# Optimization experiments

Measured on AMD Instinct MI355X. Metric: run time of the kernel, lower is better.

Reference implementation:

```python
import jax, jax.numpy as jnp
import numpy as np

N, D, R, T, E = 4096, 1024, 92, 32, 8192
SCALE = float(np.sqrt(2.0 / 7.0))  # matches torch.rand(...) * sqrt(2/7)


def setup_inputs() -> dict:
    key = jax.random.key(0)
    ks = jax.random.split(key, 7)
    x = jax.random.normal(ks[0], (N, D), dtype=jnp.float32)
    edge_tok = jax.random.randint(ks[1], (E,), 0, N)
    edge_rel = jax.random.randint(ks[2], (E,), 0, R)
    W_stack = jax.random.uniform(ks[3], (R, D, D), dtype=jnp.float32) * SCALE  # depWeights
    B_stack = jnp.ones((R, D), dtype=jnp.float32)                              # depBias
    W_self = jax.random.uniform(ks[4], (D, D), dtype=jnp.float32) * SCALE      # self.weight
    b_self = jnp.ones((D,), dtype=jnp.float32)                                 # self.bias
    W_tag = jax.random.normal(ks[5], (D, T), dtype=jnp.float32) * 0.02         # hidden2tag
    b_tag = jnp.zeros((T,), dtype=jnp.float32)
    return {"x": x, "W_self": W_self, "b_self": b_self, "W_stack": W_stack,
            "B_stack": B_stack, "W_tag": W_tag, "b_tag": b_tag,
            "edge_tok": edge_tok, "edge_rel": edge_rel}


def reference(x, W_self, b_self, W_stack, B_stack, W_tag, b_tag, edge_tok, edge_rel):
    n, r = x.shape[0], W_stack.shape[0]
    # C[i, r] = number of dependency edges of token i with relation r
    C = jnp.zeros((n, r), dtype=x.dtype).at[edge_tok, edge_rel].add(jnp.asarray(1.0, x.dtype))
    self_out = x @ W_self + b_self  # [N, D]
    # accum_i = self_out_i + sum_{dep in deps(i)} (x_i @ W_dep + b_dep)
    #         = self_out_i + sum_r C[i, r] * (x_i @ W_r) + (C @ B_stack)_i
    def body(acc, wc):
        Wr, Cr = wc  # Wr: [D, D], Cr: [N]
        return acc + Cr[:, None] * (x @ Wr), None
    dep_out, _ = jax.lax.scan(body, jnp.zeros_like(self_out), (W_stack, C.T))
    h = jax.nn.relu(self_out + dep_out + C @ B_stack)  # [N, D]
    tag_scores = jax.nn.log_softmax(h @ W_tag + b_tag, axis=1)  # [N, T]
    return tag_scores, h
```

## Files before the change

### kernel.cpp

```cpp
#include <hip/hip_runtime.h>
#include <hip/hip_bf16.h>
#include <math.h>

#define N_TOK 4096
#define D_DIM 1024
#define R_REL 92
#define T_TAG 32
#define E_EDGE 8192
#define SELF_R 127
#define GRID_ITEMS 192


typedef short bf16x8 __attribute__((ext_vector_type(8)));
typedef float f32x4 __attribute__((ext_vector_type(4)));

union Pk8 { uint4 q; unsigned short s[8]; };
union Pk4 { uint2 d; unsigned short s[4]; };

__device__ __forceinline__ unsigned short f2bf(float f) {
    union { __hip_bfloat16 b; unsigned short u; } c;
    c.b = __float2bfloat16(f);
    return c.u;
}
__device__ __forceinline__ float bf2f(unsigned short u) {
    return __uint_as_float(((unsigned)u) << 16);
}

__global__ __launch_bounds__(1024) void k_setup(const int* __restrict__ rel,
                                                const int* __restrict__ tokv,
                                                int* __restrict__ ws) {
    __shared__ int cnt[128], offL[128], cur[128];
    __shared__ int sh[128];
    __shared__ int wsum[16];
    __shared__ int tcnt[4096], toff[4096];
    int t = threadIdx.x;
    int lane = t & 63, wid = t >> 6;
    if (t < 128) { cnt[t] = 0; cur[t] = 0; }
    #pragma unroll
    for (int i = 0; i < 4; ++i) tcnt[i * 1024 + t] = 0;
    __syncthreads();
    int er[8], et[8];
    #pragma unroll
    for (int i = 0; i < 8; ++i) {
        er[i] = rel[i * 1024 + t];
        et[i] = tokv[i * 1024 + t];
        atomicAdd(&cnt[er[i]], 1);
        atomicAdd(&tcnt[et[i]], 1);
    }
    __syncthreads();
    int c = (t < 128) ? cnt[t] : 0;
    int v = c;
    if (t < 128) sh[t] = v;
    __syncthreads();
    for (int st = 1; st < 128; st <<= 1) {
        int add = (t >= st && t < 128) ? sh[t - st] : 0;
        __syncthreads();
        if (t < 128) { v += add; sh[t] = v; }
        __syncthreads();
    }
    if (t < 128) { offL[t] = v - c; ws[256 + t] = v - c; ws[t] = c; }
    int ch = (t < R_REL) ? ((c + 127) >> 7) : 0;
    int v2 = ch;
    if (t < 128) sh[t] = v2;
    __syncthreads();
    for (int st = 1; st < 128; st <<= 1) {
        int add = (t >= st && t < 128) ? sh[t - st] : 0;
        __syncthreads();
        if (t < 128) { v2 += add; sh[t] = v2; }
        __syncthreads();
    }
    if (t < 32) ws[512 + t] = (SELF_R << 16) | t;
    if (t < R_REL) {
        int excl = v2 - ch;
        for (int j = 0; j < ch; ++j)
            ws[512 + 32 + excl + j] = (t << 16) | j;
    }
    if (t == 127) ws[384] = 32 + v2;
    int s0 = tcnt[4 * t + 0], s1 = tcnt[4 * t + 1];
    int s2 = tcnt[4 * t + 2], s3 = tcnt[4 * t + 3];
    int sum4 = s0 + s1 + s2 + s3;
    int vv = sum4;
    #pragma unroll
    for (int d = 1; d < 64; d <<= 1) {
        int n = __shfl_up(vv, d);
        if (lane >= d) vv += n;
    }
    if (lane == 63) wsum[wid] = vv;
    __syncthreads();
    if (wid == 0) {
        int wv = (lane < 16) ? wsum[lane] : 0;
        #pragma unroll
        for (int d = 1; d < 16; d <<= 1) {
            int n = __shfl_up(wv, d);
            if (lane >= d) wv += n;
        }
        if (lane < 16) wsum[lane] = wv;
    }
    __syncthreads();
    int base = (wid > 0) ? wsum[wid - 1] : 0;
    int incl = base + vv;
    int ex = incl - sum4;
    toff[4 * t + 0] = ex;
    toff[4 * t + 1] = ex + s0;
    toff[4 * t + 2] = ex + s0 + s1;
    toff[4 * t + 3] = ex + s0 + s1 + s2;
    ws[17408 + 4 * t + 0] = ex;
    ws[17408 + 4 * t + 1] = ex + s0;
    ws[17408 + 4 * t + 2] = ex + s0 + s1;
    ws[17408 + 4 * t + 3] = ex + s0 + s1 + s2;
    if (t == 1023) ws[17408 + 4096] = incl;
    __syncthreads();
    #pragma unroll
    for (int i = 0; i < 4; ++i) tcnt[i * 1024 + t] = 0;
    __syncthreads();
    #pragma unroll
    for (int i = 0; i < 8; ++i) {
        int pos = offL[er[i]] + atomicAdd(&cur[er[i]], 1);
        ws[1024 + pos] = et[i];
        int q = toff[et[i]] + atomicAdd(&tcnt[et[i]], 1);
        ws[22528 + q] = pos;
    }
}

__global__ __launch_bounds__(256, 2) void k_fused(const float* __restrict__ x,
                                                  const float* __restrict__ Wself,
                                                  const float* __restrict__ bself,
                                                  const float* __restrict__ Wst,
                                                  const float* __restrict__ Bst,
                                                  const int* __restrict__ ws,
                                                  unsigned short* __restrict__ scratch) {
    if ((int)blockIdx.x >= ws[384]) return;
    int item = ws[512 + blockIdx.x];
    int r = item >> 16, chunk = item & 0xFFFF;
    int m0 = chunk * 128;
    int valid;
    const float* Wbase;
    const float* bias;
    bool is_self = (r == SELF_R);
    int off0 = 0;
    if (is_self) {
        valid = 128;
        Wbase = Wself;
        bias = bself;
    } else {
        int cnt = ws[r];
        off0 = ws[256 + r];
        valid = cnt - m0; if (valid > 128) valid = 128;
        Wbase = Wst + (size_t)r * D_DIM * D_DIM;
        bias = Bst + (size_t)r * D_DIM;
    }
    int srow_base = is_self ? (8192 + m0) : (off0 + m0);

    __shared__ unsigned short Al[2][128 * 64];
    __shared__ unsigned short Bl[2][128 * 64];
    __shared__ int toks[128];
    int t = threadIdx.x;
    if (t < 128) {
        int tok;
        if (is_self) tok = m0 + t;
        else tok = (t < valid) ? ws[1024 + off0 + m0 + t] : 0;
        toks[t] = tok;
    }
    __syncthreads();

    int gn0 = blockIdx.y * 128;
    int w = t >> 6, l = t & 63;
    int lr = l & 15, lg = l >> 4;
    int wm = (w >> 1) * 64, wn = (w & 1) * 64;
    int ar = t >> 4, ac = t & 15;
    int tok_s[8];
    #pragma unroll
    for (int s = 0; s < 8; ++s) tok_s[s] = toks[s * 16 + ar];
    int bn = (w & 1) * 64 + l;
    int bkb = (w >> 1) * 32;
    const float* wcol = Wbase + gn0 + bn;

    float4 pa[8];
    float pb[32];

    #pragma unroll
    for (int s = 0; s < 8; ++s)
        pa[s] = *(const float4*)(x + (size_t)tok_s[s] * D_DIM + ac * 4);
    #pragma unroll
    for (int s = 0; s < 4; ++s)
        #pragma unroll
        for (int i = 0; i < 8; ++i)
            pb[s * 8 + i] = wcol[(size_t)(bkb + s * 8 + i) * D_DIM];
    {
        char* Ab = (char*)Al[0];
        char* Bb = (char*)Bl[0];
        #pragma unroll
        for (int s = 0; s < 8; ++s) {
            int row = s * 16 + ar;
            Pk4 u;
            u.s[0] = f2bf(pa[s].x); u.s[1] = f2bf(pa[s].y);
            u.s[2] = f2bf(pa[s].z); u.s[3] = f2bf(pa[s].w);
            *(uint2*)(Ab + row * 128 + ((ac * 8) ^ ((row & 7) << 4))) = u.d;
        }
        #pragma unroll
        for (int s = 0; s < 4; ++s) {
            Pk8 u;
            #pragma unroll
            for (int i = 0; i < 8; ++i) u.s[i] = f2bf(pb[s * 8 + i]);
            *(uint4*)(Bb + bn * 128 + ((bkb * 2 + s * 16) ^ ((bn & 7) << 4))) = u.q;
        }
    }
    __syncthreads();

    f32x4 acc[4][4] = {};
    int cur = 0;
    for (int k0 = 0; k0 < D_DIM; k0 += 64) {
        bool pf = (k0 + 64 < D_DIM);
        if (pf) {
            int kn = k0 + 64;
            #pragma unroll
            for (int s = 0; s < 8; ++s)
                pa[s] = *(const float4*)(x + (size_t)tok_s[s] * D_DIM + kn + ac * 4);
            #pragma unroll
            for (int s = 0; s < 4; ++s)
                #pragma unroll
                for (int i = 0; i < 8; ++i)
                    pb[s * 8 + i] = wcol[(size_t)(kn + bkb + s * 8 + i) * D_DIM];
        }
        char* Ac = (char*)Al[cur];
        char* Bc = (char*)Bl[cur];
        #pragma unroll
        for (int kk = 0; kk < 2; ++kk) {
            int koff = kk * 64 + lg * 16;
            bf16x8 af[4], bfr[4];
            #pragma unroll
            for (int mi = 0; mi < 4; ++mi)
                af[mi] = *(const bf16x8*)(Ac + (wm + mi * 16 + lr) * 128 +
                                          (koff ^ ((lr & 7) << 4)));
            #pragma unroll
            for (int ni = 0; ni < 4; ++ni)
                bfr[ni] = *(const bf16x8*)(Bc + (wn + ni * 16 + lr) * 128 +
                                           (koff ^ ((lr & 7) << 4)));
            #pragma unroll
            for (int mi = 0; mi < 4; ++mi)
                #pragma unroll
                for (int ni = 0; ni < 4; ++ni)
                    acc[mi][ni] = __builtin_amdgcn_mfma_f32_16x16x32_bf16(
                        af[mi], bfr[ni], acc[mi][ni], 0, 0, 0);
        }
        if (pf) {
            char* An = (char*)Al[cur ^ 1];
            char* Bn = (char*)Bl[cur ^ 1];
            #pragma unroll
            for (int s = 0; s < 8; ++s) {
                int row = s * 16 + ar;
                Pk4 u;
                u.s[0] = f2bf(pa[s].x); u.s[1] = f2bf(pa[s].y);
                u.s[2] = f2bf(pa[s].z); u.s[3] = f2bf(pa[s].w);
                *(uint2*)(An + row * 128 + ((ac * 8) ^ ((row & 7) << 4))) = u.d;
            }
            #pragma unroll
            for (int s = 0; s < 4; ++s) {
                Pk8 u;
                #pragma unroll
                for (int i = 0; i < 8; ++i) u.s[i] = f2bf(pb[s * 8 + i]);
                *(uint4*)(Bn + bn * 128 + ((bkb * 2 + s * 16) ^ ((bn & 7) << 4))) = u.q;
            }
        }
        __syncthreads();
        cur ^= 1;
    }
    float bb[4];
    #pragma unroll
    for (int ni = 0; ni < 4; ++ni) bb[ni] = bias[gn0 + wn + ni * 16 + lr];
    #pragma unroll
    for (int mi = 0; mi < 4; ++mi)
        #pragma unroll
        for (int j = 0; j < 4; ++j) {
            int rl = wm + mi * 16 + lg * 4 + j;
            if (rl < valid) {
                unsigned short* dst = scratch +
                    (size_t)(srow_base + rl) * D_DIM + gn0 + wn + lr;
                #pragma unroll
                for (int ni = 0; ni < 4; ++ni)
                    dst[ni * 16] = f2bf(acc[mi][ni][j] + bb[ni]);
            }
        }
}

__global__ __launch_bounds__(256) void k_reduce(const int* __restrict__ ws,
                                                const unsigned short* __restrict__ scratch,
                                                float* __restrict__ out_h) {
    int tok = blockIdx.x;
    int t = threadIdx.x;
    int j0 = ws[17408 + tok], j1 = ws[17408 + tok + 1];
    ushort4 sv = *(const ushort4*)(scratch + (size_t)(8192 + tok) * D_DIM + t * 4);
    float a0 = bf2f(sv.x), a1 = bf2f(sv.y), a2 = bf2f(sv.z), a3 = bf2f(sv.w);
    for (int j = j0; j < j1; ++j) {
        int p = ws[22528 + j];
        ushort4 dv = *(const ushort4*)(scratch + (size_t)p * D_DIM + t * 4);
        a0 += bf2f(dv.x); a1 += bf2f(dv.y); a2 += bf2f(dv.z); a3 += bf2f(dv.w);
    }
    float4 o;
    o.x = fmaxf(a0, 0.f); o.y = fmaxf(a1, 0.f);
    o.z = fmaxf(a2, 0.f); o.w = fmaxf(a3, 0.f);
    *(float4*)(out_h + (size_t)tok * D_DIM + t * 4) = o;
}

__global__ __launch_bounds__(256) void k_tag(const float* __restrict__ out_h,
                                             const float* __restrict__ Wt,
                                             const float* __restrict__ bt,
                                             float* __restrict__ out_tag) {
    __shared__ unsigned short Al[64 * 64];
    __shared__ unsigned short Bl[32 * 64];
    char* Alb = (char*)Al;
    char* Blb = (char*)Bl;
    int tok0 = blockIdx.x * 64;
    int t = threadIdx.x;
    int w = t >> 6, l = t & 63, lr = l & 15, lg = l >> 4;
    int wm = w * 16;
    int ar = t >> 4, ac = t & 15;
    int bn = t & 31, kh = t >> 5;
    f32x4 acc[2] = {};
    for (int k0 = 0; k0 < D_DIM; k0 += 64) {
        __syncthreads();
        #pragma unroll
        for (int s = 0; s < 4; ++s) {
            int row = s * 16 + ar;
            const float* hp = out_h + (size_t)(tok0 + row) * D_DIM + k0 + ac * 4;
            float4 v = *(const float4*)hp;
            Pk4 u;
            u.s[0] = f2bf(v.x); u.s[1] = f2bf(v.y);
            u.s[2] = f2bf(v.z); u.s[3] = f2bf(v.w);
            *(uint2*)(Alb + row * 128 + ((ac * 8) ^ ((row & 7) << 4))) = u.d;
        }
        {
            Pk8 u;
            #pragma unroll
            for (int i = 0; i < 8; ++i)
                u.s[i] = f2bf(Wt[(size_t)(k0 + kh * 8 + i) * T_TAG + bn]);
            *(uint4*)(Blb + bn * 128 + ((kh * 16) ^ ((bn & 7) << 4))) = u.q;
        }
        __syncthreads();
        #pragma unroll
        for (int kk = 0; kk < 2; ++kk) {
            int koff = kk * 64 + lg * 16;
            bf16x8 af = *(const bf16x8*)(Alb + (wm + lr) * 128 +
                                         (koff ^ ((lr & 7) << 4)));
            #pragma unroll
            for (int ni = 0; ni < 2; ++ni) {
                bf16x8 bfr = *(const bf16x8*)(Blb + (ni * 16 + lr) * 128 +
                                              (koff ^ ((lr & 7) << 4)));
                acc[ni] = __builtin_amdgcn_mfma_f32_16x16x32_bf16(
                    af, bfr, acc[ni], 0, 0, 0);
            }
        }
    }
    float bt0 = bt[lr], bt1 = bt[16 + lr];
    #pragma unroll
    for (int j = 0; j < 4; ++j) {
        float v0 = acc[0][j] + bt0;
        float v1 = acc[1][j] + bt1;
        float m = fmaxf(v0, v1);
        #pragma unroll
        for (int s = 1; s < 16; s <<= 1) m = fmaxf(m, __shfl_xor(m, s));
        float sum = expf(v0 - m) + expf(v1 - m);
        #pragma unroll
        for (int s = 1; s < 16; s <<= 1) sum += __shfl_xor(sum, s);
        float lse = m + logf(sum);
        int row = tok0 + wm + lg * 4 + j;
        out_tag[(size_t)row * T_TAG + lr] = v0 - lse;
        out_tag[(size_t)row * T_TAG + 16 + lr] = v1 - lse;
    }
}

extern "C" void kernel_launch(void* const* d_in, const int* in_sizes, int n_in,
                              void* d_out, int out_size, void* d_ws, size_t ws_size,
                              hipStream_t stream) {
    const float* x     = (const float*)d_in[0];
    const float* Wself = (const float*)d_in[1];
    const float* bself = (const float*)d_in[2];
    const float* Wst   = (const float*)d_in[3];
    const float* Bst   = (const float*)d_in[4];
    const float* Wtag  = (const float*)d_in[5];
    const float* btag  = (const float*)d_in[6];
    const int*   etok  = (const int*)d_in[7];
    const int*   erel  = (const int*)d_in[8];
    float* out_tag = (float*)d_out;
    float* out_h   = (float*)d_out + (size_t)N_TOK * T_TAG;
    int* ws = (int*)d_ws;
    unsigned short* scratch = (unsigned short*)((int*)d_ws + 32768);

    k_setup<<<1, 1024, 0, stream>>>(erel, etok, ws);
    k_fused<<<dim3(GRID_ITEMS, D_DIM / 128), 256, 0, stream>>>(
        x, Wself, bself, Wst, Bst, ws, scratch);
    k_reduce<<<N_TOK, 256, 0, stream>>>(ws, scratch, out_h);
    k_tag<<<N_TOK / 64, 256, 0, stream>>>(out_h, Wtag, btag, out_tag);
}
```

Before: 149.4 us.

## Pre-convert x to bf16 and stream A tiles via direct global-to-LDS loads

Adds blocks to the setup kernel that convert x to a bf16 copy in workspace, so the GEMM kernel can gather token rows with global_load_lds straight into swizzled shared memory instead of loading fp32 into registers and converting. The GEMM block grows from 256 to 512 threads with an 8-wave 2x4 layout (each wave computes 64x32), which halves per-thread B loads and accumulators and raises the occupancy hint. This removes register staging and conversion work for A in the main loop, at the cost of an extra pass over x and more waves sharing LDS and barriers.

```diff
diff --git a/kernel.cpp b/kernel.cpp
--- a/kernel.cpp
+++ b/kernel.cpp
@@ -25,15 +25,34 @@
 __device__ __forceinline__ float bf2f(unsigned short u) {
     return __uint_as_float(((unsigned)u) << 16);
 }
-
-__global__ __launch_bounds__(1024) void k_setup(const int* __restrict__ rel,
-                                                const int* __restrict__ tokv,
-                                                int* __restrict__ ws) {
+__device__ __forceinline__ void gload_lds16(const void* g, void* l) {
+    __builtin_amdgcn_global_load_lds(
+        (const __attribute__((address_space(1))) unsigned int*)g,
+        (__attribute__((address_space(3))) unsigned int*)l, 16, 0, 0);
+}
+
+__global__ __launch_bounds__(1024) void k_prep(const int* __restrict__ rel,
+                                               const int* __restrict__ tokv,
+                                               const float* __restrict__ x,
+                                               int* __restrict__ ws,
+                                               unsigned short* __restrict__ xb) {
+    int t = threadIdx.x;
+    if (blockIdx.x > 0) {
+        size_t base = ((size_t)(blockIdx.x - 1) * 1024 + t) * 8;
+        float4 v0 = *(const float4*)(x + base);
+        float4 v1 = *(const float4*)(x + base + 4);
+        Pk8 u;
+        u.s[0] = f2bf(v0.x); u.s[1] = f2bf(v0.y);
+        u.s[2] = f2bf(v0.z); u.s[3] = f2bf(v0.w);
+        u.s[4] = f2bf(v1.x); u.s[5] = f2bf(v1.y);
+        u.s[6] = f2bf(v1.z); u.s[7] = f2bf(v1.w);
+        *(uint4*)(xb + base) = u.q;
+        return;
+    }
     __shared__ int cnt[128], offL[128], cur[128];
     __shared__ int sh[128];
     __shared__ int wsum[16];
     __shared__ int tcnt[4096], toff[4096];
-    int t = threadIdx.x;
     int lane = t & 63, wid = t >> 6;
     if (t < 128) { cnt[t] = 0; cur[t] = 0; }
     #pragma unroll
@@ -122,12 +141,12 @@
     }
 }
 
-__global__ __launch_bounds__(256, 2) void k_fused(const float* __restrict__ x,
-                                                  const float* __restrict__ Wself,
+__global__ __launch_bounds__(512, 4) void k_fused(const float* __restrict__ Wself,
                                                   const float* __restrict__ bself,
                                                   const float* __restrict__ Wst,
                                                   const float* __restrict__ Bst,
                                                   const int* __restrict__ ws,
+                                                  const unsigned short* __restrict__ xb,
                                                   unsigned short* __restrict__ scratch) {
     if ((int)blockIdx.x >= ws[384]) return;
     int item = ws[512 + blockIdx.x];
@@ -151,8 +170,8 @@
     }
     int srow_base = is_self ? (8192 + m0) : (off0 + m0);
 
-    __shared__ unsigned short Al[2][128 * 64];
-    __shared__ unsigned short Bl[2][128 * 64];
+    __shared__ unsigned short Al[2][8192];
+    __shared__ unsigned short Bl[2][8192];
     __shared__ int toks[128];
     int t = threadIdx.x;
     if (t < 128) {
@@ -164,110 +183,84 @@
     __syncthreads();
 
     int gn0 = blockIdx.y * 128;
-    int w = t >> 6, l = t & 63;
+    int wid = t >> 6, l = t & 63;
     int lr = l & 15, lg = l >> 4;
-    int wm = (w >> 1) * 64, wn = (w & 1) * 64;
-    int ar = t >> 4, ac = t & 15;
-    int tok_s[8];
-    #pragma unroll
-    for (int s = 0; s < 8; ++s) tok_s[s] = toks[s * 16 + ar];
-    int bn = (w & 1) * 64 + l;
-    int bkb = (w >> 1) * 32;
-    const float* wcol = Wbase + gn0 + bn;
-
-    float4 pa[8];
-    float pb[32];
-
-    #pragma unroll
-    for (int s = 0; s < 8; ++s)
-        pa[s] = *(const float4*)(x + (size_t)tok_s[s] * D_DIM + ac * 4);
-    #pragma unroll
-    for (int s = 0; s < 4; ++s)
-        #pragma unroll
-        for (int i = 0; i < 8; ++i)
-            pb[s * 8 + i] = wcol[(size_t)(bkb + s * 8 + i) * D_DIM];
+    int wm = (wid >> 2) * 64, wn = (wid & 3) * 32;
+
+    int row0 = wid * 16 + (l >> 3);
+    int row1 = row0 + 8;
+    const char* ga0 = (const char*)(xb + (size_t)toks[row0] * D_DIM) +
+                      (((l & 7) * 16) ^ ((row0 & 7) << 4));
+    const char* ga1 = (const char*)(xb + (size_t)toks[row1] * D_DIM) +
+                      (((l & 7) * 16) ^ ((row1 & 7) << 4));
+
+    int bcol = t & 127, bkq = t >> 7;
+    const float* wp = Wbase + (size_t)bkq * 16 * D_DIM + gn0 + bcol;
+    int bswz = (bcol & 7) << 4;
+    int bb0 = bcol * 128 + ((bkq * 32) ^ bswz);
+    int bb1 = bcol * 128 + ((bkq * 32 + 16) ^ bswz);
+
+    float pb[16];
+    gload_lds16(ga0, (char*)Al[0] + wid * 2048);
+    gload_lds16(ga1, (char*)Al[0] + wid * 2048 + 1024);
+    ga0 += 128; ga1 += 128;
+    #pragma unroll
+    for (int i = 0; i < 16; ++i) pb[i] = wp[(size_t)i * D_DIM];
     {
-        char* Ab = (char*)Al[0];
-        char* Bb = (char*)Bl[0];
-        #pragma unroll
-        for (int s = 0; s < 8; ++s) {
-            int row = s * 16 + ar;
-            Pk4 u;
-            u.s[0] = f2bf(pa[s].x); u.s[1] = f2bf(pa[s].y);
-            u.s[2] = f2bf(pa[s].z); u.s[3] = f2bf(pa[s].w);
-            *(uint2*)(Ab + row * 128 + ((ac * 8) ^ ((row & 7) << 4))) = u.d;
-        }
-        #pragma unroll
-        for (int s = 0; s < 4; ++s) {
-            Pk8 u;
-            #pragma unroll
-            for (int i = 0; i < 8; ++i) u.s[i] = f2bf(pb[s * 8 + i]);
-            *(uint4*)(Bb + bn * 128 + ((bkb * 2 + s * 16) ^ ((bn & 7) << 4))) = u.q;
-        }
-    }
-    __syncthreads();
-
-    f32x4 acc[4][4] = {};
+        Pk8 u0, u1;
+        #pragma unroll
+        for (int i = 0; i < 8; ++i) { u0.s[i] = f2bf(pb[i]); u1.s[i] = f2bf(pb[8 + i]); }
+        *(uint4*)((char*)Bl[0] + bb0) = u0.q;
+        *(uint4*)((char*)Bl[0] + bb1) = u1.q;
+    }
+    __syncthreads();
+
+    f32x4 acc[4][2] = {};
     int cur = 0;
     for (int k0 = 0; k0 < D_DIM; k0 += 64) {
         bool pf = (k0 + 64 < D_DIM);
+        int nxt = cur ^ 1;
         if (pf) {
-            int kn = k0 + 64;
-            #pragma unroll
-            for (int s = 0; s < 8; ++s)
-                pa[s] = *(const float4*)(x + (size_t)tok_s[s] * D_DIM + kn + ac * 4);
-            #pragma unroll
-            for (int s = 0; s < 4; ++s)
-                #pragma unroll
-                for (int i = 0; i < 8; ++i)
-                    pb[s * 8 + i] = wcol[(size_t)(kn + bkb + s * 8 + i) * D_DIM];
-        }
-        char* Ac = (char*)Al[cur];
-        char* Bc = (char*)Bl[cur];
+            gload_lds16(ga0, (char*)Al[nxt] + wid * 2048);
+            gload_lds16(ga1, (char*)Al[nxt] + wid * 2048 + 1024);
+            ga0 += 128; ga1 += 128;
+            #pragma unroll
+            for (int i = 0; i < 16; ++i)
+                pb[i] = wp[(size_t)(k0 + 64 + i) * D_DIM];
+        }
+        const char* Ac = (const char*)Al[cur];
+        const char* Bc = (const char*)Bl[cur];
         #pragma unroll
         for (int kk = 0; kk < 2; ++kk) {
             int koff = kk * 64 + lg * 16;
-            bf16x8 af[4], bfr[4];
+            int sw = (lr & 7) << 4;
+            bf16x8 af[4], bfr[2];
             #pragma unroll
             for (int mi = 0; mi < 4; ++mi)
-                af[mi] = *(const bf16x8*)(Ac + (wm + mi * 16 + lr) * 128 +
-                                          (koff ^ ((lr & 7) << 4)));
-            #pragma unroll
-            for (int ni = 0; ni < 4; ++ni)
-                bfr[ni] = *(const bf16x8*)(Bc + (wn + ni * 16 + lr) * 128 +
-                                           (koff ^ ((lr & 7) << 4)));
+                af[mi] = *(const bf16x8*)(Ac + (wm + mi * 16 + lr) * 128 + (koff ^ sw));
+            #pragma unroll
+            for (int ni = 0; ni < 2; ++ni)
+                bfr[ni] = *(const bf16x8*)(Bc + (wn + ni * 16 + lr) * 128 + (koff ^ sw));
             #pragma unroll
             for (int mi = 0; mi < 4; ++mi)
                 #pragma unroll
-                for (int ni = 0; ni < 4; ++ni)
+                for (int ni = 0; ni < 2; ++ni)
                     acc[mi][ni] = __builtin_amdgcn_mfma_f32_16x16x32_bf16(
                         af[mi], bfr[ni], acc[mi][ni], 0, 0, 0);
         }
         if (pf) {
-            char* An = (char*)Al[cur ^ 1];
-            char* Bn = (char*)Bl[cur ^ 1];
-            #pragma unroll
-            for (int s = 0; s < 8; ++s) {
-                int row = s * 16 + ar;
-                Pk4 u;
-                u.s[0] = f2bf(pa[s].x); u.s[1] = f2bf(pa[s].y);
-                u.s[2] = f2bf(pa[s].z); u.s[3] = f2bf(pa[s].w);
-                *(uint2*)(An + row * 128 + ((ac * 8) ^ ((row & 7) << 4))) = u.d;
-            }
-            #pragma unroll
-            for (int s = 0; s < 4; ++s) {
-                Pk8 u;
-                #pragma unroll
-                for (int i = 0; i < 8; ++i) u.s[i] = f2bf(pb[s * 8 + i]);
-                *(uint4*)(Bn + bn * 128 + ((bkb * 2 + s * 16) ^ ((bn & 7) << 4))) = u.q;
-            }
-        }
-        __syncthreads();
-        cur ^= 1;
-    }
-    float bb[4];
-    #pragma unroll
-    for (int ni = 0; ni < 4; ++ni) bb[ni] = bias[gn0 + wn + ni * 16 + lr];
+            Pk8 u0, u1;
+            #pragma unroll
+            for (int i = 0; i < 8; ++i) { u0.s[i] = f2bf(pb[i]); u1.s[i] = f2bf(pb[8 + i]); }
+            *(uint4*)((char*)Bl[nxt] + bb0) = u0.q;
+            *(uint4*)((char*)Bl[nxt] + bb1) = u1.q;
+        }
+        __syncthreads();
+        cur = nxt;
+    }
+    float bb[2];
+    bb[0] = bias[gn0 + wn + lr];
+    bb[1] = bias[gn0 + wn + 16 + lr];
     #pragma unroll
     for (int mi = 0; mi < 4; ++mi)
         #pragma unroll
@@ -276,9 +269,8 @@
             if (rl < valid) {
                 unsigned short* dst = scratch +
                     (size_t)(srow_base + rl) * D_DIM + gn0 + wn + lr;
-                #pragma unroll
-                for (int ni = 0; ni < 4; ++ni)
-                    dst[ni * 16] = f2bf(acc[mi][ni][j] + bb[ni]);
+                dst[0]  = f2bf(acc[mi][0][j] + bb[0]);
+                dst[16] = f2bf(acc[mi][1][j] + bb[1]);
             }
         }
 }
@@ -385,10 +377,11 @@
     float* out_h   = (float*)d_out + (size_t)N_TOK * T_TAG;
     int* ws = (int*)d_ws;
     unsigned short* scratch = (unsigned short*)((int*)d_ws + 32768);
-
-    k_setup<<<1, 1024, 0, stream>>>(erel, etok, ws);
-    k_fused<<<dim3(GRID_ITEMS, D_DIM / 128), 256, 0, stream>>>(
-        x, Wself, bself, Wst, Bst, ws, scratch);
+    unsigned short* xb = scratch + (size_t)12288 * 1024;
+
+    k_prep<<<513, 1024, 0, stream>>>(erel, etok, x, ws, xb);
+    k_fused<<<dim3(GRID_ITEMS, D_DIM / 128), 512, 0, stream>>>(
+        Wself, bself, Wst, Bst, ws, xb, scratch);
     k_reduce<<<N_TOK, 256, 0, stream>>>(ws, scratch, out_h);
     k_tag<<<N_TOK / 64, 256, 0, stream>>>(out_h, Wtag, btag, out_tag);
 }
```

Result: faster. 144.6 us (-3.2%).
